# Kernel tuning notes

Hardware: AMD Instinct MI355X
Metric: run time of the kernel (lower is better)

Reference implementation:

```python
import jax, jax.numpy as jnp
import numpy as np

D_EMBED = 1024
N_HEADS = 16
D_HEAD = 64
D_MLP = 4096
SEQ = 2048
BATCH = 2
ALPHA = 1.0


def setup_inputs() -> dict:
    key = jax.random.key(0)
    ks = jax.random.split(key, 7)
    s = ALPHA / np.sqrt(D_EMBED)
    return {
        "x": jax.random.normal(ks[0], (BATCH, SEQ, D_EMBED), jnp.float32),
        "W_K": s * jax.random.normal(ks[1], (N_HEADS, D_HEAD, D_EMBED), jnp.float32),
        "W_Q": s * jax.random.normal(ks[2], (N_HEADS, D_HEAD, D_EMBED), jnp.float32),
        "W_V": s * jax.random.normal(ks[3], (N_HEADS, D_HEAD, D_EMBED), jnp.float32),
        "W_O": s * jax.random.normal(ks[4], (D_EMBED, N_HEADS * D_HEAD), jnp.float32),
        "W_in": s * jax.random.normal(ks[5], (D_MLP, D_EMBED), jnp.float32),
        "b_in": jnp.zeros((D_MLP,), jnp.float32),
        "W_out": s * jax.random.normal(ks[6], (D_EMBED, D_MLP), jnp.float32),
        "b_out": jnp.zeros((D_EMBED,), jnp.float32),
    }


def reference(x, W_K, W_Q, W_V, W_O, W_in, b_in, W_out, b_out):
    b, c_len, _ = x.shape
    d_head = W_K.shape[1]
    # q/k/v: [batch, head, ctx, d_head]
    k = jnp.einsum('ahe,bce->bach', W_K, x)
    q = jnp.einsum('ahe,bce->bach', W_Q, x)
    v = jnp.einsum('ahe,bce->bach', W_V, x)
    # scores[b,a,c,C] = k_c . q_C  (faithful to original index convention)
    scores = jnp.einsum('bach,baCh->bacC', k, q)
    mask = jnp.tril(jnp.ones((c_len, c_len), dtype=x.dtype))  # [c, C]
    masked = scores * mask - 1e10 * (1.0 - mask)
    attn = jax.nn.softmax(masked / np.sqrt(d_head), axis=-1)  # softmax over C (query idx)
    # z[b,a,C,h] = sum_c v[b,a,c,h] * attn[b,a,c,C]
    z = jnp.einsum('bach,bacC->baCh', v, attn)
    z_flat = jnp.transpose(z, (0, 2, 1, 3)).reshape(b, c_len, -1)  # [b, c, a*h]
    attn_out = jnp.einsum('ef,bcf->bce', W_O, z_flat)
    x = x + attn_out
    h = jnp.einsum('me,bce->bcm', W_in, x) + b_in
    h = jax.nn.relu(h)
    mlp_out = jnp.einsum('em,bcm->bce', W_out, h) + b_out
    return x + mlp_out
```

## Files before the change

kernel.cpp:

```cpp
#include <hip/hip_runtime.h>
#include <hip/hip_bf16.h>
#include <cstdint>
#include <cstddef>

typedef __bf16 bf16;
typedef bf16 bf16x4 __attribute__((ext_vector_type(4)));
typedef bf16 bf16x8 __attribute__((ext_vector_type(8)));
typedef float floatx4 __attribute__((ext_vector_type(4)));
typedef float floatx16 __attribute__((ext_vector_type(16)));
typedef unsigned int uint;

#define MFMA16(a, b, c) __builtin_amdgcn_mfma_f32_16x16x32_bf16((a), (b), (c), 0, 0, 0)
#define MFMA32(a, b, c) __builtin_amdgcn_mfma_f32_32x32x16_bf16((a), (b), (c), 0, 0, 0)

#define K2 0.18033688011112042f

__device__ __forceinline__ void async16(const void* g, void* l) {
    __builtin_amdgcn_global_load_lds((const __attribute__((address_space(1))) void*)g,
                                     (__attribute__((address_space(3))) void*)l,
                                     16, 0, 0);
}

__device__ __forceinline__ void stage64s(const bf16* g0, int ldg, bf16* lds, int wave, int lane) {
#pragma unroll
    for (int i = 0; i < 2; ++i) {
        int r0 = wave * 16 + i * 8;
        async16(g0 + (size_t)(r0 + (lane >> 3)) * ldg + ((lane & 7) ^ (lane >> 3)) * 8,
                lds + r0 * 64);
    }
}
__device__ __forceinline__ void stage64q(const bf16* g0, int ldg, bf16* lds, int wave, int lane) {
    int r0 = wave * 8;
    async16(g0 + (size_t)(r0 + (lane >> 3)) * ldg + ((lane & 7) ^ (lane >> 3)) * 8,
            lds + r0 * 64);
}
__device__ __forceinline__ bf16x8 rd64(const bf16* t, int row, int chunk) {
    return *(const bf16x8*)&t[row * 64 + ((chunk ^ (row & 7)) * 8)];
}
__device__ __forceinline__ bf16x8 rd32(const bf16* t, int row, int quad) {
    return *(const bf16x8*)&t[row * 32 + ((quad ^ (row & 3)) * 8)];
}

__device__ __forceinline__ uint pk2(float lo, float hi) {
    union { bf16 h[2]; uint u; } c;
    c.h[0] = (bf16)lo;
    c.h[1] = (bf16)hi;
    return c.u;
}

__global__ __launch_bounds__(256) void cvt_all(const float* __restrict__ x,
                                               const float* __restrict__ WQ,
                                               const float* __restrict__ WK,
                                               const float* __restrict__ WV,
                                               const float* __restrict__ WO,
                                               const float* __restrict__ Win,
                                               const float* __restrict__ Wout,
                                               bf16* __restrict__ xb,
                                               bf16* __restrict__ wqkv,
                                               bf16* __restrict__ wo,
                                               bf16* __restrict__ win,
                                               bf16* __restrict__ wout) {
    int blk = blockIdx.x;
    const float* src;
    bf16* dst;
    int off;
    if (blk < 1024)      { src = WQ;   dst = wqkv;           off = blk; }
    else if (blk < 2048) { src = WK;   dst = wqkv + 1048576; off = blk - 1024; }
    else if (blk < 3072) { src = WV;   dst = wqkv + 2097152; off = blk - 2048; }
    else if (blk < 4096) { src = WO;   dst = wo;             off = blk - 3072; }
    else if (blk < 8192) { src = Win;  dst = win;            off = blk - 4096; }
    else if (blk < 12288){ src = Wout; dst = wout;           off = blk - 8192; }
    else                 { src = x;    dst = xb;             off = blk - 12288; }
    int i = off * 1024 + threadIdx.x * 4;
    float4 v = *(const float4*)(src + i);
    bf16x4 o = {(bf16)v.x, (bf16)v.y, (bf16)v.z, (bf16)v.w};
    *(bf16x4*)(dst + i) = o;
}

template <int EPI, int NACC>
__device__ __forceinline__ void epilogue(floatx4 (&acc)[4][NACC], int m0, int n0,
                                         int wm, int wn, int col, int quad,
                                         float* Cf, bf16* Cb, int ldc,
                                         const float* bias, const float* res) {
#pragma unroll
    for (int mi = 0; mi < 4; ++mi)
#pragma unroll
        for (int ni = 0; ni < NACC; ++ni)
#pragma unroll
            for (int r = 0; r < 4; ++r) {
                int row = m0 + wm + mi * 16 + quad * 4 + r;
                int cc = n0 + wn + ni * 16 + col;
                size_t idx = (size_t)row * ldc + cc;
                float v = acc[mi][ni][r];
                if constexpr (EPI == 0) {
                    Cb[idx] = (bf16)v;
                } else if constexpr (EPI == 1) {
                    v += res[idx];
                    Cf[idx] = v;
                    Cb[idx] = (bf16)v;
                } else if constexpr (EPI == 2) {
                    v += bias[cc];
                    v = fmaxf(v, 0.f);
                    Cb[idx] = (bf16)v;
                } else {
                    v += bias[cc] + Cf[idx];
                    Cf[idx] = v;
                }
            }
}

template <int EPI>
__global__ __launch_bounds__(256) void gemm_pipe(const bf16* __restrict__ A, int lda,
                                                 const bf16* __restrict__ B, int ldb, int K,
                                                 float* __restrict__ Cf, bf16* __restrict__ Cb,
                                                 int ldc, const float* __restrict__ bias,
                                                 const float* __restrict__ res) {
    __shared__ __align__(16) bf16 As[3][128 * 32];
    __shared__ __align__(16) bf16 Bs[3][128 * 32];
    const int tid = threadIdx.x, wave = tid >> 6, lane = tid & 63;
    const int m0 = blockIdx.y * 128, n0 = blockIdx.x * 128;
    const int wm = (wave >> 1) * 64, wn = (wave & 1) * 64;
    const int col = lane & 15, quad = lane >> 4;
    const int cs8 = ((lane & 3) ^ ((lane >> 2) & 3)) * 8;

    floatx4 acc[4][4];
#pragma unroll
    for (int mi = 0; mi < 4; ++mi)
#pragma unroll
        for (int ni = 0; ni < 4; ++ni) acc[mi][ni] = (floatx4){0.f, 0.f, 0.f, 0.f};

    auto stage = [&](int buf, int k0) {
#pragma unroll
        for (int i = 0; i < 2; ++i) {
            int r0 = wave * 32 + i * 16;
            async16(A + (size_t)(m0 + r0 + (lane >> 2)) * lda + k0 + cs8,
                    As[buf] + r0 * 32);
            async16(B + (size_t)(n0 + r0 + (lane >> 2)) * ldb + k0 + cs8,
                    Bs[buf] + r0 * 32);
        }
    };

    const int nk = K / 32;
    stage(0, 0);
    stage(1, 32);
    for (int it = 0; it < nk; ++it) {
        if (it + 1 < nk) asm volatile("s_waitcnt vmcnt(4)" ::: "memory");
        else             asm volatile("s_waitcnt vmcnt(0)" ::: "memory");
        __builtin_amdgcn_s_barrier();
        if (it + 2 < nk) stage((it + 2) % 3, (it + 2) * 32);

        const bf16* as = As[it % 3];
        const bf16* bs = Bs[it % 3];
        bf16x8 af[4], bfr[4];
#pragma unroll
        for (int mi = 0; mi < 4; ++mi) af[mi] = rd32(as, wm + mi * 16 + col, quad);
#pragma unroll
        for (int ni = 0; ni < 4; ++ni) bfr[ni] = rd32(bs, wn + ni * 16 + col, quad);
#pragma unroll
        for (int mi = 0; mi < 4; ++mi)
#pragma unroll
            for (int ni = 0; ni < 4; ++ni)
                acc[mi][ni] = MFMA16(af[mi], bfr[ni], acc[mi][ni]);
    }
    epilogue<EPI, 4>(acc, m0, n0, wm, wn, col, quad, Cf, Cb, ldc, bias, res);
}

template <int EPI>
__global__ __launch_bounds__(512, 2) void gemm_8p(const bf16* __restrict__ A, int lda,
                                                  const bf16* __restrict__ B, int ldb, int K,
                                                  float* __restrict__ Cf, bf16* __restrict__ Cb,
                                                  int ldc, const float* __restrict__ bias,
                                                  const float* __restrict__ res) {
    __shared__ __align__(16) bf16 As[3][256 * 32];
    __shared__ __align__(16) bf16 Bs[3][256 * 32];
    const int tid = threadIdx.x, wave = tid >> 6, lane = tid & 63;
    const int gx = gridDim.x;
    const int orig = blockIdx.y * gx + blockIdx.x;
    const int cpx = (gx * gridDim.y) >> 3;
    const int swz = (orig & 7) * cpx + (orig >> 3);
    const int m0 = (swz % gx) * 256, n0 = (swz / gx) * 256;
    const int wm = (wave >> 2) * 128, wn = (wave & 3) * 64;
    const int col = lane & 15, quad = lane >> 4;
    const int cs8 = ((lane & 3) ^ ((lane >> 2) & 3)) * 8;

    floatx4 acc[8][4];
#pragma unroll
    for (int mi = 0; mi < 8; ++mi)
#pragma unroll
        for (int ni = 0; ni < 4; ++ni) acc[mi][ni] = (floatx4){0.f, 0.f, 0.f, 0.f};

    auto stageA = [&](int buf, int k0) {
#pragma unroll
        for (int i = 0; i < 2; ++i) {
            int r0 = wave * 32 + i * 16;
            async16(A + (size_t)(m0 + r0 + (lane >> 2)) * lda + k0 + cs8,
                    As[buf] + r0 * 32);
        }
    };
    auto stageB = [&](int buf, int k0) {
#pragma unroll
        for (int i = 0; i < 2; ++i) {
            int r0 = wave * 32 + i * 16;
            async16(B + (size_t)(n0 + r0 + (lane >> 2)) * ldb + k0 + cs8,
                    Bs[buf] + r0 * 32);
        }
    };

    const int nk = K / 32;
    stageA(0, 0); stageB(0, 0);
    stageA(1, 32); stageB(1, 32);
    for (int it = 0; it < nk; ++it) {
        if (it + 1 < nk) asm volatile("s_waitcnt vmcnt(4)" ::: "memory");
        else             asm volatile("s_waitcnt vmcnt(0)" ::: "memory");
        __builtin_amdgcn_s_barrier();

        const bf16* as = As[it % 3];
        const bf16* bs = Bs[it % 3];
        const int pb = (it + 2) % 3;
        const int pk = (it + 2) * 32;

        if (it + 2 < nk) stageA(pb, pk);
        bf16x8 bfr[4];
#pragma unroll
        for (int ni = 0; ni < 4; ++ni) bfr[ni] = rd32(bs, wn + ni * 16 + col, quad);
        {
            bf16x8 af[4];
#pragma unroll
            for (int mi = 0; mi < 4; ++mi) af[mi] = rd32(as, wm + mi * 16 + col, quad);
            __builtin_amdgcn_s_setprio(1);
#pragma unroll
            for (int mi = 0; mi < 4; ++mi)
#pragma unroll
                for (int ni = 0; ni < 4; ++ni)
                    acc[mi][ni] = MFMA16(af[mi], bfr[ni], acc[mi][ni]);
            __builtin_amdgcn_s_setprio(0);
        }
        __builtin_amdgcn_s_barrier();

        if (it + 2 < nk) stageB(pb, pk);
        {
            bf16x8 af[4];
#pragma unroll
            for (int mi = 0; mi < 4; ++mi)
                af[mi] = rd32(as, wm + 64 + mi * 16 + col, quad);
            __builtin_amdgcn_s_setprio(1);
#pragma unroll
            for (int mi = 0; mi < 4; ++mi)
#pragma unroll
                for (int ni = 0; ni < 4; ++ni)
                    acc[mi + 4][ni] = MFMA16(af[mi], bfr[ni], acc[mi + 4][ni]);
            __builtin_amdgcn_s_setprio(0);
        }
    }

#pragma unroll
    for (int mi = 0; mi < 8; ++mi)
#pragma unroll
        for (int ni = 0; ni < 4; ++ni)
#pragma unroll
            for (int r = 0; r < 4; ++r) {
                int row = m0 + wm + mi * 16 + quad * 4 + r;
                int cc = n0 + wn + ni * 16 + col;
                size_t idx = (size_t)row * ldc + cc;
                float v = acc[mi][ni][r];
                if constexpr (EPI == 2) {
                    v += bias[cc];
                    v = fmaxf(v, 0.f);
                    Cb[idx] = (bf16)v;
                } else {
                    Cb[idx] = (bf16)v;
                }
            }
    (void)Cf; (void)res;
}

template <int EPI>
__global__ __launch_bounds__(256) void gemm_pipe64(const bf16* __restrict__ A, int lda,
                                                   const bf16* __restrict__ B, int ldb, int K,
                                                   float* __restrict__ Cf, bf16* __restrict__ Cb,
                                                   int ldc, const float* __restrict__ bias,
                                                   const float* __restrict__ res) {
    __shared__ __align__(16) bf16 As[3][128 * 64];
    __shared__ __align__(16) bf16 Bs[3][64 * 64];
    const int tid = threadIdx.x, wave = tid >> 6, lane = tid & 63;
    const int orig = blockIdx.y * 16 + blockIdx.x;
    const int wgid = (orig & 7) * 64 + (orig >> 3);
    const int m0 = (wgid >> 4) * 128, n0 = (wgid & 15) * 64;
    const int wm = (wave >> 1) * 64, wn = (wave & 1) * 32;
    const int col = lane & 15, quad = lane >> 4;
    const int rsub = lane >> 3;
    const int csub = ((lane & 7) ^ rsub) * 8;

    floatx4 acc[4][2];
#pragma unroll
    for (int mi = 0; mi < 4; ++mi)
#pragma unroll
        for (int ni = 0; ni < 2; ++ni) acc[mi][ni] = (floatx4){0.f, 0.f, 0.f, 0.f};

    auto stage = [&](int buf, int k0) {
#pragma unroll
        for (int i = 0; i < 4; ++i) {
            int r0 = wave * 32 + i * 8;
            async16(A + (size_t)(m0 + r0 + rsub) * lda + k0 + csub, As[buf] + r0 * 64);
        }
#pragma unroll
        for (int i = 0; i < 2; ++i) {
            int r0 = wave * 16 + i * 8;
            async16(B + (size_t)(n0 + r0 + rsub) * ldb + k0 + csub, Bs[buf] + r0 * 64);
        }
    };

    const int nk = K / 64;
    stage(0, 0);
    stage(1, 64);
    for (int it = 0; it < nk; ++it) {
        if (it + 1 < nk) asm volatile("s_waitcnt vmcnt(6)" ::: "memory");
        else             asm volatile("s_waitcnt vmcnt(0)" ::: "memory");
        __builtin_amdgcn_s_barrier();
        if (it + 2 < nk) stage((it + 2) % 3, (it + 2) * 64);

        const bf16* as = As[it % 3];
        const bf16* bs = Bs[it % 3];
#pragma unroll
        for (int ks = 0; ks < 2; ++ks) {
            bf16x8 af[4], bfr[2];
#pragma unroll
            for (int mi = 0; mi < 4; ++mi) {
                int row = wm + mi * 16 + col;
                af[mi] = *(const bf16x8*)&as[row * 64 + (((ks * 4 + quad) ^ (row & 7)) * 8)];
            }
#pragma unroll
            for (int ni = 0; ni < 2; ++ni) {
                int row = wn + ni * 16 + col;
                bfr[ni] = *(const bf16x8*)&bs[row * 64 + (((ks * 4 + quad) ^ (row & 7)) * 8)];
            }
#pragma unroll
            for (int mi = 0; mi < 4; ++mi)
#pragma unroll
                for (int ni = 0; ni < 2; ++ni)
                    acc[mi][ni] = MFMA16(af[mi], bfr[ni], acc[mi][ni]);
        }
    }
    epilogue<EPI, 2>(acc, m0, n0, wm, wn, col, quad, Cf, Cb, ldc, bias, res);
}

__global__ __launch_bounds__(256) void transpose_v(const bf16* __restrict__ qkv,
                                                   const float* __restrict__ linv,
                                                   bf16* __restrict__ vt) {
    __shared__ bf16 t[64][65];
    const int bh = blockIdx.y, ct = blockIdx.x;
    const int b = bh >> 4, a = bh & 15;
    const float* lv = linv + (size_t)bh * 2048 + ct * 64;
    for (int idx = threadIdx.x; idx < 4096; idx += 256) {
        int c = idx >> 6, h = idx & 63;
        float v = (float)qkv[(size_t)(b * 2048 + ct * 64 + c) * 3072 + 2048 + a * 64 + h];
        t[h][c] = (bf16)(v * lv[c]);
    }
    __syncthreads();
    for (int idx = threadIdx.x; idx < 4096; idx += 256) {
        int h = idx >> 6, c = idx & 63;
        vt[(size_t)(bh * 64 + h) * 2048 + ct * 64 + c] = t[h][c];
    }
}

__global__ __launch_bounds__(512, 4) void attn_stats(const bf16* __restrict__ qkv,
                                                     float* __restrict__ linv) {
    __shared__ __align__(16) bf16 Kt[128 * 64];
    __shared__ __align__(16) bf16 Qt[3][64 * 64];
    __shared__ float red[4][32];
    const int xx = blockIdx.x;
    const int t = (xx & 1) ? (15 - (xx >> 1)) : (xx >> 1);
    const int bh = blockIdx.y;
    const int b = bh >> 4, a = bh & 15;
    const int tid = threadIdx.x, wave = tid >> 6, lane = tid & 63;
    const int l31 = lane & 31, lh = lane >> 5;
    const int kq = wave & 3, qh = wave >> 2;
    const bf16* base = qkv + (size_t)b * 2048 * 3072;
    const int c0 = t * 128;
    const int niter = 2 * t + 2;

    stage64s(base + (size_t)c0 * 3072 + 1024 + a * 64, 3072, Kt, wave, lane);
    stage64q(base + a * 64, 3072, Qt[0], wave, lane);
    stage64q(base + (size_t)64 * 3072 + a * 64, 3072, Qt[1], wave, lane);

    float lrun[16];
#pragma unroll
    for (int r = 0; r < 16; ++r) lrun[r] = 0.f;
    bf16x8 kf[4];

    for (int i = 0; i < niter; ++i) {
        if (i + 1 < niter) asm volatile("s_waitcnt vmcnt(1)" ::: "memory");
        else               asm volatile("s_waitcnt vmcnt(0)" ::: "memory");
        __builtin_amdgcn_s_barrier();
        if (i + 2 < niter)
            stage64q(base + (size_t)(i + 2) * 64 * 3072 + a * 64, 3072,
                     Qt[(i + 2) % 3], wave, lane);
        if (i == 0) {
#pragma unroll
            for (int s = 0; s < 4; ++s) kf[s] = rd64(Kt, 32 * kq + l31, 2 * s + lh);
        }
        const bf16* q = Qt[i % 3];
        bf16x8 qf0 = rd64(q, 32 * qh + l31, 0 + lh);
        bf16x8 qf1 = rd64(q, 32 * qh + l31, 2 + lh);
        bf16x8 qf2 = rd64(q, 32 * qh + l31, 4 + lh);
        bf16x8 qf3 = rd64(q, 32 * qh + l31, 6 + lh);
        floatx16 s0 = (floatx16)0.f, s1 = (floatx16)0.f;
        __builtin_amdgcn_s_setprio(1);
        s0 = MFMA32(kf[0], qf0, s0);
        s1 = MFMA32(kf[2], qf2, s1);
        s0 = MFMA32(kf[1], qf1, s0);
        s1 = MFMA32(kf[3], qf3, s1);
        __builtin_amdgcn_s_setprio(0);
#pragma unroll
        for (int r = 0; r < 16; ++r) {
            float e = __builtin_amdgcn_exp2f((s0[r] + s1[r]) * K2);
            if (i >= niter - 2) {
                int Crel = 64 * (i - 2 * t) + 32 * qh + l31;
                int crel = 32 * kq + (r & 3) + 8 * (r >> 2) + 4 * lh;
                if (Crel > crel) e = 0.f;
            }
            lrun[r] += e;
        }
    }
#pragma unroll
    for (int r = 0; r < 16; ++r) {
        float v = lrun[r];
        v += __shfl_xor(v, 1);
        v += __shfl_xor(v, 2);
        v += __shfl_xor(v, 4);
        v += __shfl_xor(v, 8);
        v += __shfl_xor(v, 16);
        lrun[r] = v;
    }
    if (qh == 1 && l31 == 0) {
#pragma unroll
        for (int r = 0; r < 16; ++r)
            red[kq][(r & 3) + 8 * (r >> 2) + 4 * lh] = lrun[r];
    }
    __syncthreads();
    if (qh == 0 && l31 == 0) {
#pragma unroll
        for (int r = 0; r < 16; ++r) {
            int cr = (r & 3) + 8 * (r >> 2) + 4 * lh;
            linv[(size_t)bh * 2048 + c0 + 32 * kq + cr] = 1.0f / (lrun[r] + red[kq][cr]);
        }
    }
}

__global__ __launch_bounds__(512, 4) void attn_av(const bf16* __restrict__ qkv,
                                                  const bf16* __restrict__ vt,
                                                  bf16* __restrict__ zb) {
    __shared__ __align__(16) char smem[65536];
    bf16* Qt = (bf16*)smem;
    bf16* Kt = (bf16*)(smem + 16384);
    bf16* Vt = (bf16*)(smem + 40960);
    const int xx = blockIdx.x;
    const int t = (xx & 1) ? (15 - (xx >> 1)) : (xx >> 1);
    const int bh = blockIdx.y;
    const int b = bh >> 4, a = bh & 15;
    const int tid = threadIdx.x, wave = tid >> 6, lane = tid & 63;
    const int l31 = lane & 31, lh = lane >> 5;
    const int Cq = wave & 3, cq = wave >> 2;
    const bf16* base = qkv + (size_t)b * 2048 * 3072;
    const int C0 = t * 128;
    const int niter = 32 - 2 * t;

    stage64s(base + (size_t)C0 * 3072 + a * 64, 3072, Qt, wave, lane);
    stage64q(base + (size_t)(2 * t) * 64 * 3072 + 1024 + a * 64, 3072, Kt, wave, lane);
    stage64q(vt + (size_t)bh * 64 * 2048 + 2 * t * 64, 2048, Vt, wave, lane);
    stage64q(base + (size_t)(2 * t + 1) * 64 * 3072 + 1024 + a * 64, 3072, Kt + 4096, wave, lane);
    stage64q(vt + (size_t)bh * 64 * 2048 + (2 * t + 1) * 64, 2048, Vt + 4096, wave, lane);

    floatx16 zacc[2];
    zacc[0] = (floatx16)0.f;
    zacc[1] = (floatx16)0.f;
    bf16x8 qf[4];

    for (int i = 0; i < niter; ++i) {
        const int ct = 2 * t + i;
        if (i + 1 < niter) asm volatile("s_waitcnt vmcnt(2)" ::: "memory");
        else               asm volatile("s_waitcnt vmcnt(0)" ::: "memory");
        __builtin_amdgcn_s_barrier();
        if (i + 2 < niter) {
            stage64q(base + (size_t)(ct + 2) * 64 * 3072 + 1024 + a * 64, 3072,
                     Kt + ((i + 2) % 3) * 4096, wave, lane);
            stage64q(vt + (size_t)bh * 64 * 2048 + (ct + 2) * 64, 2048,
                     Vt + ((i + 2) % 3) * 4096, wave, lane);
        }
        if (i == 0) {
#pragma unroll
            for (int s = 0; s < 4; ++s) qf[s] = rd64(Qt, 32 * Cq + l31, 2 * s + lh);
        }
        const bf16* kt = Kt + (i % 3) * 4096;
        const bf16* vts = Vt + (i % 3) * 4096;

        floatx16 s0 = (floatx16)0.f, s1 = (floatx16)0.f;
        __builtin_amdgcn_s_setprio(1);
        s0 = MFMA32(rd64(kt, 32 * cq + l31, 0 + lh), qf[0], s0);
        s1 = MFMA32(rd64(kt, 32 * cq + l31, 4 + lh), qf[2], s1);
        s0 = MFMA32(rd64(kt, 32 * cq + l31, 2 + lh), qf[1], s0);
        s1 = MFMA32(rd64(kt, 32 * cq + l31, 6 + lh), qf[3], s1);
        __builtin_amdgcn_s_setprio(0);

        float p[16];
#pragma unroll
        for (int r = 0; r < 16; ++r) {
            float e = __builtin_amdgcn_exp2f((s0[r] + s1[r]) * K2);
            if (i < 2) {
                int Crel = 32 * Cq + l31;
                int crel = 64 * i + 32 * cq + (r & 3) + 8 * (r >> 2) + 4 * lh;
                if (Crel > crel) e = 0.f;
            }
            p[r] = e;
        }

        bf16x8 pa[2];
#pragma unroll
        for (int g = 0; g < 2; ++g) {
            uint w0 = pk2(p[8 * g + 0], p[8 * g + 1]);
            uint w1 = pk2(p[8 * g + 2], p[8 * g + 3]);
            uint w2 = pk2(p[8 * g + 4], p[8 * g + 5]);
            uint w3 = pk2(p[8 * g + 6], p[8 * g + 7]);
            uint xw0 = (uint)__shfl_xor((int)w0, 32);
            uint xw1 = (uint)__shfl_xor((int)w1, 32);
            uint xw2 = (uint)__shfl_xor((int)w2, 32);
            uint xw3 = (uint)__shfl_xor((int)w3, 32);
            union { uint u[4]; bf16x8 v; } cv;
            cv.u[0] = lh ? xw2 : w0;
            cv.u[1] = lh ? xw3 : w1;
            cv.u[2] = lh ? w2 : xw0;
            cv.u[3] = lh ? w3 : xw1;
            pa[g] = cv.v;
        }

        __builtin_amdgcn_s_setprio(1);
#pragma unroll
        for (int ht = 0; ht < 2; ++ht) {
#pragma unroll
            for (int s = 0; s < 2; ++s) {
                bf16x8 vf = rd64(vts, 32 * ht + l31, 4 * cq + 2 * s + lh);
                zacc[ht] = MFMA32(pa[s], vf, zacc[ht]);
            }
        }
        __builtin_amdgcn_s_setprio(0);
    }

    __syncthreads();
    float* Zex = (float*)smem;
    if (cq == 1) {
#pragma unroll
        for (int ht = 0; ht < 2; ++ht)
#pragma unroll
            for (int q = 0; q < 4; ++q) {
                float4 t4 = {zacc[ht][4 * q + 0], zacc[ht][4 * q + 1],
                             zacc[ht][4 * q + 2], zacc[ht][4 * q + 3]};
                *(float4*)&Zex[Cq * 2048 + lane * 32 + (((ht * 4 + q) ^ (lane & 7)) * 4)] = t4;
            }
    }
    __syncthreads();
    if (cq == 0) {
#pragma unroll
        for (int ht = 0; ht < 2; ++ht)
#pragma unroll
            for (int q = 0; q < 4; ++q) {
                float4 t4 = *(const float4*)&Zex[Cq * 2048 + lane * 32 +
                                                 (((ht * 4 + q) ^ (lane & 7)) * 4)];
                zacc[ht][4 * q + 0] += t4.x;
                zacc[ht][4 * q + 1] += t4.y;
                zacc[ht][4 * q + 2] += t4.z;
                zacc[ht][4 * q + 3] += t4.w;
            }
#pragma unroll
        for (int ht = 0; ht < 2; ++ht)
#pragma unroll
            for (int r = 0; r < 16; ++r) {
                int Cg = C0 + 32 * Cq + (r & 3) + 8 * (r >> 2) + 4 * lh;
                zb[(size_t)(b * 2048 + Cg) * 1024 + a * 64 + 32 * ht + l31] =
                    (bf16)zacc[ht][r];
            }
    }
}

extern "C" void kernel_launch(void* const* d_in, const int* in_sizes, int n_in,
                              void* d_out, int out_size, void* d_ws, size_t ws_size,
                              hipStream_t stream) {
    (void)in_sizes; (void)n_in; (void)out_size; (void)ws_size;
    const float* x    = (const float*)d_in[0];
    const float* WK   = (const float*)d_in[1];
    const float* WQ   = (const float*)d_in[2];
    const float* WV   = (const float*)d_in[3];
    const float* WO   = (const float*)d_in[4];
    const float* Win  = (const float*)d_in[5];
    const float* bin  = (const float*)d_in[6];
    const float* Wout = (const float*)d_in[7];
    const float* bout = (const float*)d_in[8];
    float* out = (float*)d_out;

    char* ws = (char*)d_ws;
    bf16*  xb   = (bf16*)(ws + 0);
    bf16*  wqkv = (bf16*)(ws + 8388608);
    bf16*  wo   = (bf16*)(ws + 14680064);
    bf16*  win  = (bf16*)(ws + 16777216);
    bf16*  wout = (bf16*)(ws + 25165824);
    bf16*  qkvb = (bf16*)(ws + 33554432);
    bf16*  vtb  = (bf16*)(ws + 58720256);
    float* mst  = (float*)(ws + 67108864);
    bf16*  zbuf = (bf16*)(ws + 67633152);
    bf16*  xmid = (bf16*)(ws + 76021760);
    bf16*  hbuf = (bf16*)(ws + 84410368);

    cvt_all<<<16384, 256, 0, stream>>>(x, WQ, WK, WV, WO, Win, Wout,
                                       xb, wqkv, wo, win, wout);

    gemm_pipe<0><<<dim3(24, 32), 256, 0, stream>>>(xb, 1024, wqkv, 1024, 1024,
                                                   nullptr, qkvb, 3072, nullptr, nullptr);
    attn_stats<<<dim3(16, 32), 512, 0, stream>>>(qkvb, mst);
    transpose_v<<<dim3(32, 32), 256, 0, stream>>>(qkvb, mst, vtb);
    attn_av<<<dim3(16, 32), 512, 0, stream>>>(qkvb, vtb, zbuf);
    gemm_pipe64<1><<<dim3(16, 32), 256, 0, stream>>>(zbuf, 1024, wo, 1024, 1024,
                                                     out, xmid, 1024, nullptr, x);
    gemm_8p<2><<<dim3(16, 16), 512, 0, stream>>>(xmid, 1024, win, 1024, 1024,
                                                 nullptr, hbuf, 4096, bin, nullptr);
    gemm_pipe64<3><<<dim3(16, 32), 256, 0, stream>>>(hbuf, 4096, wout, 4096, 4096,
                                                     out, nullptr, 1024, bout, nullptr);
}
```

Before: 375.0 us.

## Split-K the MLP down-projection with 256x256 tiles and a reduction kernel

The final MLP GEMM (K=4096, N=1024) moves from the 128x64-tile pipelined kernel to the 256x256 8-wave kernel, split into four K-chunks along blockIdx.z. Each chunk writes a bf16 partial into a reused workspace region, and a new elementwise kernel sums the four partials and adds the bias and residual into the output. This aims to get larger-tile MFMA efficiency while keeping 256 workgroups in flight. The cost is an extra kernel launch and partial-sum traffic, and rounding partials to bf16 loses some accuracy.

```diff
diff --git a/kernel.cpp b/kernel.cpp
--- a/kernel.cpp
+++ b/kernel.cpp
@@ -179,6 +179,9 @@
     const int cpx = (gx * gridDim.y) >> 3;
     const int swz = (orig & 7) * cpx + (orig >> 3);
     const int m0 = (swz % gx) * 256, n0 = (swz / gx) * 256;
+    A += (size_t)blockIdx.z * K;
+    B += (size_t)blockIdx.z * K;
+    Cb += (size_t)blockIdx.z * (size_t)gx * 256 * ldc;
     const int wm = (wave >> 2) * 128, wn = (wave & 3) * 64;
     const int col = lane & 15, quad = lane >> 4;
     const int cs8 = ((lane & 3) ^ ((lane >> 2) & 3)) * 8;
@@ -272,6 +275,28 @@
                 }
             }
     (void)Cf; (void)res;
+}
+
+__global__ __launch_bounds__(256) void mlp2_reduce(const bf16* __restrict__ p,
+                                                   const float* __restrict__ bout,
+                                                   float* __restrict__ out) {
+    int i = (blockIdx.x * 256 + threadIdx.x) * 4;
+    float4 o = *(const float4*)(out + i);
+    float4 bb = *(const float4*)(bout + (i & 1023));
+    float s0 = 0.f, s1 = 0.f, s2 = 0.f, s3 = 0.f;
+#pragma unroll
+    for (int z = 0; z < 4; ++z) {
+        bf16x4 v = *(const bf16x4*)(p + (size_t)z * 4194304 + i);
+        s0 += (float)v[0];
+        s1 += (float)v[1];
+        s2 += (float)v[2];
+        s3 += (float)v[3];
+    }
+    o.x += s0 + bb.x;
+    o.y += s1 + bb.y;
+    o.z += s2 + bb.z;
+    o.w += s3 + bb.w;
+    *(float4*)(out + i) = o;
 }
 
 template <int EPI>
@@ -608,6 +633,7 @@
     bf16*  zbuf = (bf16*)(ws + 67633152);
     bf16*  xmid = (bf16*)(ws + 76021760);
     bf16*  hbuf = (bf16*)(ws + 84410368);
+    bf16*  partb = (bf16*)(ws + 33554432);
 
     cvt_all<<<16384, 256, 0, stream>>>(x, WQ, WK, WV, WO, Win, Wout,
                                        xb, wqkv, wo, win, wout);
@@ -621,6 +647,7 @@
                                                      out, xmid, 1024, nullptr, x);
     gemm_8p<2><<<dim3(16, 16), 512, 0, stream>>>(xmid, 1024, win, 1024, 1024,
                                                  nullptr, hbuf, 4096, bin, nullptr);
-    gemm_pipe64<3><<<dim3(16, 32), 256, 0, stream>>>(hbuf, 4096, wout, 4096, 4096,
-                                                     out, nullptr, 1024, bout, nullptr);
-}
+    gemm_8p<0><<<dim3(16, 4, 4), 512, 0, stream>>>(hbuf, 4096, wout, 4096, 1024,
+                                                   nullptr, partb, 1024, nullptr, nullptr);
+    mlp2_reduce<<<4096, 256, 0, stream>>>(partb, bout, out);
+}
```

Result: slower. 385.7 us (+2.9%).

## Restructure MLP-in GEMM into double-buffered 64-deep K pipeline with split waits

Applied to the files above, without the earlier changes.

Replaces the triple-buffered 32-wide K pipeline of the 256x256 MLP-up GEMM with a double-buffered scheme that loads 64 K per stage as two 32-wide halves. Each half's A and B tiles are issued interleaved with four MFMA phases, with explicit lgkmcnt and vmcnt waits and extra barriers. The aim is to halve the outer iteration count and overlap global-to-LDS loads with compute more finely. LDS use rises from 96KB to 128KB per block, and the added barriers may cost more sync overhead. Only this one GEMM in the chain of kernels changes.

```diff
diff --git a/kernel.cpp b/kernel.cpp
--- a/kernel.cpp
+++ b/kernel.cpp
@@ -166,13 +166,12 @@
 }
 
 template <int EPI>
-__global__ __launch_bounds__(512, 2) void gemm_8p(const bf16* __restrict__ A, int lda,
-                                                  const bf16* __restrict__ B, int ldb, int K,
-                                                  float* __restrict__ Cf, bf16* __restrict__ Cb,
-                                                  int ldc, const float* __restrict__ bias,
-                                                  const float* __restrict__ res) {
-    __shared__ __align__(16) bf16 As[3][256 * 32];
-    __shared__ __align__(16) bf16 Bs[3][256 * 32];
+__global__ __launch_bounds__(512, 2) void gemm_deep(const bf16* __restrict__ A, int lda,
+                                                    const bf16* __restrict__ B, int ldb, int K,
+                                                    bf16* __restrict__ Cb, int ldc,
+                                                    const float* __restrict__ bias) {
+    __shared__ __align__(16) bf16 As[2][2][256 * 32];
+    __shared__ __align__(16) bf16 Bs[2][2][256 * 32];
     const int tid = threadIdx.x, wave = tid >> 6, lane = tid & 63;
     const int gx = gridDim.x;
     const int orig = blockIdx.y * gx + blockIdx.x;
@@ -189,68 +188,101 @@
 #pragma unroll
         for (int ni = 0; ni < 4; ++ni) acc[mi][ni] = (floatx4){0.f, 0.f, 0.f, 0.f};
 
-    auto stageA = [&](int buf, int k0) {
+    auto stA = [&](int buf, int kh, int kb) {
 #pragma unroll
         for (int i = 0; i < 2; ++i) {
             int r0 = wave * 32 + i * 16;
-            async16(A + (size_t)(m0 + r0 + (lane >> 2)) * lda + k0 + cs8,
-                    As[buf] + r0 * 32);
+            async16(A + (size_t)(m0 + r0 + (lane >> 2)) * lda + kb + kh * 32 + cs8,
+                    As[buf][kh] + r0 * 32);
         }
     };
-    auto stageB = [&](int buf, int k0) {
+    auto stB = [&](int buf, int kh, int kb) {
 #pragma unroll
         for (int i = 0; i < 2; ++i) {
             int r0 = wave * 32 + i * 16;
-            async16(B + (size_t)(n0 + r0 + (lane >> 2)) * ldb + k0 + cs8,
-                    Bs[buf] + r0 * 32);
+            async16(B + (size_t)(n0 + r0 + (lane >> 2)) * ldb + kb + kh * 32 + cs8,
+                    Bs[buf][kh] + r0 * 32);
         }
     };
 
-    const int nk = K / 32;
-    stageA(0, 0); stageB(0, 0);
-    stageA(1, 32); stageB(1, 32);
-    for (int it = 0; it < nk; ++it) {
-        if (it + 1 < nk) asm volatile("s_waitcnt vmcnt(4)" ::: "memory");
-        else             asm volatile("s_waitcnt vmcnt(0)" ::: "memory");
-        __builtin_amdgcn_s_barrier();
-
-        const bf16* as = As[it % 3];
-        const bf16* bs = Bs[it % 3];
-        const int pb = (it + 2) % 3;
-        const int pk = (it + 2) * 32;
-
-        if (it + 2 < nk) stageA(pb, pk);
-        bf16x8 bfr[4];
-#pragma unroll
-        for (int ni = 0; ni < 4; ++ni) bfr[ni] = rd32(bs, wn + ni * 16 + col, quad);
-        {
-            bf16x8 af[4];
-#pragma unroll
-            for (int mi = 0; mi < 4; ++mi) af[mi] = rd32(as, wm + mi * 16 + col, quad);
-            __builtin_amdgcn_s_setprio(1);
-#pragma unroll
-            for (int mi = 0; mi < 4; ++mi)
-#pragma unroll
-                for (int ni = 0; ni < 4; ++ni)
-                    acc[mi][ni] = MFMA16(af[mi], bfr[ni], acc[mi][ni]);
-            __builtin_amdgcn_s_setprio(0);
-        }
-        __builtin_amdgcn_s_barrier();
-
-        if (it + 2 < nk) stageB(pb, pk);
-        {
-            bf16x8 af[4];
-#pragma unroll
-            for (int mi = 0; mi < 4; ++mi)
-                af[mi] = rd32(as, wm + 64 + mi * 16 + col, quad);
-            __builtin_amdgcn_s_setprio(1);
-#pragma unroll
-            for (int mi = 0; mi < 4; ++mi)
-#pragma unroll
-                for (int ni = 0; ni < 4; ++ni)
-                    acc[mi + 4][ni] = MFMA16(af[mi], bfr[ni], acc[mi + 4][ni]);
-            __builtin_amdgcn_s_setprio(0);
-        }
+    const int nk = K / 64;
+    stA(0, 0, 0); stB(0, 0, 0); stA(0, 1, 0); stB(0, 1, 0);
+    asm volatile("s_waitcnt vmcnt(4)" ::: "memory");
+    __builtin_amdgcn_s_barrier();
+
+    for (int t = 0; t < nk; ++t) {
+        const int c = t & 1, nb = c ^ 1;
+        const bf16* a0 = As[c][0];
+        const bf16* a1 = As[c][1];
+        const bf16* b0s = Bs[c][0];
+        const bf16* b1s = Bs[c][1];
+        const int kb1 = (t + 1) * 64;
+        const bool pre = (t + 1 < nk);
+        bf16x8 bfr[4], af[4];
+
+        if (pre) stA(nb, 0, kb1);
+#pragma unroll
+        for (int ni = 0; ni < 4; ++ni) bfr[ni] = rd32(b0s, wn + ni * 16 + col, quad);
+#pragma unroll
+        for (int mi = 0; mi < 4; ++mi) af[mi] = rd32(a0, wm + mi * 16 + col, quad);
+        __builtin_amdgcn_s_barrier();
+        asm volatile("s_waitcnt lgkmcnt(0)" ::: "memory");
+        __builtin_amdgcn_s_setprio(1);
+#pragma unroll
+        for (int mi = 0; mi < 4; ++mi)
+#pragma unroll
+            for (int ni = 0; ni < 4; ++ni)
+                acc[mi][ni] = MFMA16(af[mi], bfr[ni], acc[mi][ni]);
+        __builtin_amdgcn_s_setprio(0);
+        __builtin_amdgcn_s_barrier();
+
+        if (pre) stB(nb, 0, kb1);
+#pragma unroll
+        for (int mi = 0; mi < 4; ++mi) af[mi] = rd32(a0, wm + 64 + mi * 16 + col, quad);
+        __builtin_amdgcn_s_barrier();
+        asm volatile("s_waitcnt lgkmcnt(0)" ::: "memory");
+        __builtin_amdgcn_s_setprio(1);
+#pragma unroll
+        for (int mi = 0; mi < 4; ++mi)
+#pragma unroll
+            for (int ni = 0; ni < 4; ++ni)
+                acc[mi + 4][ni] = MFMA16(af[mi], bfr[ni], acc[mi + 4][ni]);
+        __builtin_amdgcn_s_setprio(0);
+        if (pre) asm volatile("s_waitcnt vmcnt(4)" ::: "memory");
+        else     asm volatile("s_waitcnt vmcnt(0)" ::: "memory");
+        __builtin_amdgcn_s_barrier();
+
+        if (pre) stA(nb, 1, kb1);
+#pragma unroll
+        for (int ni = 0; ni < 4; ++ni) bfr[ni] = rd32(b1s, wn + ni * 16 + col, quad);
+#pragma unroll
+        for (int mi = 0; mi < 4; ++mi) af[mi] = rd32(a1, wm + mi * 16 + col, quad);
+        __builtin_amdgcn_s_barrier();
+        asm volatile("s_waitcnt lgkmcnt(0)" ::: "memory");
+        __builtin_amdgcn_s_setprio(1);
+#pragma unroll
+        for (int mi = 0; mi < 4; ++mi)
+#pragma unroll
+            for (int ni = 0; ni < 4; ++ni)
+                acc[mi][ni] = MFMA16(af[mi], bfr[ni], acc[mi][ni]);
+        __builtin_amdgcn_s_setprio(0);
+        __builtin_amdgcn_s_barrier();
+
+        if (pre) stB(nb, 1, kb1);
+#pragma unroll
+        for (int mi = 0; mi < 4; ++mi) af[mi] = rd32(a1, wm + 64 + mi * 16 + col, quad);
+        __builtin_amdgcn_s_barrier();
+        asm volatile("s_waitcnt lgkmcnt(0)" ::: "memory");
+        __builtin_amdgcn_s_setprio(1);
+#pragma unroll
+        for (int mi = 0; mi < 4; ++mi)
+#pragma unroll
+            for (int ni = 0; ni < 4; ++ni)
+                acc[mi + 4][ni] = MFMA16(af[mi], bfr[ni], acc[mi + 4][ni]);
+        __builtin_amdgcn_s_setprio(0);
+        if (pre) asm volatile("s_waitcnt vmcnt(4)" ::: "memory");
+        else     asm volatile("s_waitcnt vmcnt(0)" ::: "memory");
+        __builtin_amdgcn_s_barrier();
     }
 
 #pragma unroll
@@ -271,7 +303,6 @@
                     Cb[idx] = (bf16)v;
                 }
             }
-    (void)Cf; (void)res;
 }
 
 template <int EPI>
@@ -619,8 +650,8 @@
     attn_av<<<dim3(16, 32), 512, 0, stream>>>(qkvb, vtb, zbuf);
     gemm_pipe64<1><<<dim3(16, 32), 256, 0, stream>>>(zbuf, 1024, wo, 1024, 1024,
                                                      out, xmid, 1024, nullptr, x);
-    gemm_8p<2><<<dim3(16, 16), 512, 0, stream>>>(xmid, 1024, win, 1024, 1024,
-                                                 nullptr, hbuf, 4096, bin, nullptr);
+    gemm_deep<2><<<dim3(16, 16), 512, 0, stream>>>(xmid, 1024, win, 1024, 1024,
+                                                   hbuf, 4096, bin);
     gemm_pipe64<3><<<dim3(16, 32), 256, 0, stream>>>(hbuf, 4096, wout, 4096, 4096,
                                                      out, nullptr, 1024, bout, nullptr);
 }
```

Measured after the change: 372.1 us. No clear change (-0.8%).
